# Kernel tuning notes

Measured on AMD Instinct MI355X. Metric: run time of the kernel, lower is better.

The kernel has to match this reference:

```python
import jax, jax.numpy as jnp
import numpy as np

NUM_SAMPLES = 64
PE_FREQS = 10
HIDDEN = 256
IN_PE = 3 + 3 * 2 * PE_FREQS  # 63


def positional_encoding(x):
    # x: [..., 3] -> [..., 63]
    freqs = 2.0 ** jnp.arange(PE_FREQS, dtype=x.dtype)  # [L]
    xb = x[..., None, :] * freqs[:, None]               # [..., L, 3]
    enc = jnp.concatenate([jnp.sin(xb), jnp.cos(xb)], axis=-1)  # [..., L, 6]
    return jnp.concatenate([x, enc.reshape(*x.shape[:-1], -1)], axis=-1)


def setup_inputs() -> dict:
    key = jax.random.key(0)
    ks = jax.random.split(key, 12)
    origins = jax.random.normal(ks[0], (2048, 3), dtype=jnp.float32)
    directions = jax.random.normal(ks[1], (2048, 3), dtype=jnp.float32)
    directions = directions / jnp.linalg.norm(directions, axis=-1, keepdims=True)

    def lin(kw, kb, fan_in, fan_out):
        s = 1.0 / np.sqrt(fan_in)
        W = jax.random.uniform(kw, (fan_in, fan_out), jnp.float32, -s, s)
        b = jax.random.uniform(kb, (fan_out,), jnp.float32, -s, s)
        return W, b

    W0, b0 = lin(ks[2], ks[3], IN_PE, HIDDEN)
    W1, b1 = lin(ks[4], ks[5], HIDDEN, HIDDEN)
    W2, b2 = lin(ks[6], ks[7], HIDDEN, HIDDEN)
    W3, b3 = lin(ks[8], ks[9], HIDDEN, 4)
    return {"origins": origins, "directions": directions,
            "near": 2.0, "far": 6.0,
            "W0": W0, "b0": b0, "W1": W1, "b1": b1,
            "W2": W2, "b2": b2, "W3": W3, "b3": b3}


def field_mlp(x, W0, b0, W1, b1, W2, b2, W3, b3):
    h = positional_encoding(x)
    h = jax.nn.relu(h @ W0 + b0)
    h = jax.nn.relu(h @ W1 + b1)
    h = jax.nn.relu(h @ W2 + b2)
    return h @ W3 + b3  # [..., 4]


def reference(origins, directions, near, far, W0, b0, W1, b1, W2, b2, W3, b3):
    near = jnp.float32(near)
    far = jnp.float32(far)
    # 1) sample generation (faithful to source, including its midpoint formula)
    boundaries = jnp.linspace(near, far, NUM_SAMPLES + 1)          # [S+1]
    midpoints = boundaries[:-1] + boundaries[1:] / 2               # [S] (as in source)
    samples = jnp.einsum('i,jk->jik', midpoints, directions)      # [B,S,3]
    locations = origins[:, None, :] + samples                      # [B,S,3]
    # 2) field eval (vectorized; equivalent to per-ray list comprehension)
    field_out = field_mlp(locations, W0, b0, W1, b1, W2, b2, W3, b3)  # [B,S,4]
    rgb = jax.nn.sigmoid(field_out[..., :3])                       # [B,S,3]
    sigma = jax.nn.relu(field_out[..., 3])                         # [B,S]
    # 3) alpha values
    delta = jnp.diff(boundaries)                                    # [S]
    alpha = 1.0 - jnp.exp(-sigma * delta)                           # [B,S]
    # 4) alpha composite: exclusive cumprod transmittance (O(N) form of source loop)
    trans = jnp.cumprod(1.0 - alpha, axis=1)
    T = jnp.concatenate([jnp.ones_like(alpha[:, :1]), trans[:, :-1]], axis=1)
    weights = T * alpha                                             # [B,S]
    return jnp.sum(weights[..., None] * rgb, axis=1)                # [B,3]
```

## Files before the change

### kernel.cpp

```cpp
#include <hip/hip_runtime.h>
#include <math.h>

typedef _Float16 h8 __attribute__((ext_vector_type(8)));
typedef _Float16 h4 __attribute__((ext_vector_type(4)));
typedef float    f4 __attribute__((ext_vector_type(4)));

#define SAMPLES 64
#define HIDDEN  256

#define OFF_W0 0
#define OFF_W1 16384
#define OFF_W2 81920
#define OFF_W3 147456

__launch_bounds__(256)
__global__ void prep_weights(const float* __restrict__ W0,
                             const float* __restrict__ W1,
                             const float* __restrict__ W2,
                             const float* __restrict__ W3,
                             _Float16* __restrict__ ws)
{
    const int ln = threadIdx.x & 63;
    const int t  = blockIdx.x * 4 + (threadIdx.x >> 6);
    if (t >= 296) return;

    const float* src; int off, kg, ct, kmax, colmax, wide;
    if (t < 32)       { src=W0; off=OFF_W0; kg=t>>4;        ct=t&15;        kmax=63;  colmax=256; wide=1; }
    else if (t < 160) { int u=t-32;  src=W1; off=OFF_W1; kg=u>>4; ct=u&15; kmax=256; colmax=256; wide=1; }
    else if (t < 288) { int u=t-160; src=W2; off=OFF_W2; kg=u>>4; ct=u&15; kmax=256; colmax=256; wide=1; }
    else              { int u=t-288; src=W3; off=OFF_W3; kg=u;    ct=0;    kmax=256; colmax=4;   wide=0; }

    const int col = ct*16 + (ln & 15);
    const int k0  = kg*32 + ((ln >> 4) << 3);
    h8 vh;
#pragma unroll
    for (int j = 0; j < 8; ++j) {
        int k = k0 + j;
        float v = (k < kmax && col < colmax) ? src[k*colmax + col] : 0.0f;
        vh[j] = (_Float16)v;
    }
    int di = wide ? ((kg*16 + ct)*64 + ln) : (kg*64 + ln);
    ((h8*)(ws + off))[di] = vh;
}

template<int NKG>
__device__ __forceinline__ void dense_layer(const _Float16* __restrict__ W,
                                            const float*    __restrict__ bias,
                                            _Float16* B, int wv, int lane,
                                            h8 (&ca)[2],
                                            const h8* __restrict__ next0,
                                            const h8* __restrict__ next1)
{
    const int q  = lane >> 4;
    const int jl = lane & 15;
    f4 acc[2][8];
#pragma unroll
    for (int cht = 0; cht < 2; ++cht)
#pragma unroll
        for (int st = 0; st < 8; ++st) acc[cht][st] = (f4){0.f, 0.f, 0.f, 0.f};

    const h8* wp = (const h8*)W;
    const h8* bp = (const h8*)B;

#pragma unroll
    for (int kg = 0; kg < NKG; ++kg) {
        h8 na[2];
        if (kg + 1 < NKG) {
#pragma unroll
            for (int cht = 0; cht < 2; ++cht)
                na[cht] = wp[((kg+1)*16 + wv*2 + cht)*64 + lane];
        } else {
            na[0] = *next0;
            na[1] = *next1;
        }
#pragma unroll
        for (int sh = 0; sh < 2; ++sh) {
            h8 bh[4];
#pragma unroll
            for (int s = 0; s < 4; ++s)
                bh[s] = bp[(kg*8 + sh*4 + s)*64 + lane];
#pragma unroll
            for (int s = 0; s < 4; ++s) {
                acc[0][sh*4+s] = __builtin_amdgcn_mfma_f32_16x16x32_f16(ca[0], bh[s], acc[0][sh*4+s], 0, 0, 0);
                acc[1][sh*4+s] = __builtin_amdgcn_mfma_f32_16x16x32_f16(ca[1], bh[s], acc[1][sh*4+s], 0, 0, 0);
            }
        }
        ca[0] = na[0]; ca[1] = na[1];
    }

    f4 bb0 = ((const f4*)bias)[wv*8 + q];
    f4 bb1 = ((const f4*)bias)[wv*8 + 4 + q];

    __syncthreads();

#pragma unroll
    for (int cht = 0; cht < 2; ++cht) {
        f4 bb = cht ? bb1 : bb0;
        int lnp = jl + 16*(cht*2 + (q >> 1));
        int jb  = (q & 1)*4;
#pragma unroll
        for (int st = 0; st < 8; ++st) {
            h4 vh;
#pragma unroll
            for (int r = 0; r < 4; ++r)
                vh[r] = (_Float16)fmaxf(acc[cht][st][r] + bb[r], 0.0f);
            *(h4*)(B + ((wv*8 + st)*64 + lnp)*8 + jb) = vh;
        }
    }
    __syncthreads();
}

__launch_bounds__(512, 2)
__global__ void nerf_fused(const float* __restrict__ origins,
                           const float* __restrict__ dirs,
                           const float* __restrict__ nearp,
                           const float* __restrict__ farp,
                           const float* __restrict__ b0,
                           const float* __restrict__ b1,
                           const float* __restrict__ b2,
                           const float* __restrict__ b3,
                           const _Float16* __restrict__ ws,
                           float* __restrict__ out,
                           int nrays)
{
    extern __shared__ _Float16 sm[];
    _Float16* B = sm;
    float* headv = (float*)(sm + 32768);

    const int tid  = threadIdx.x;
    const int wv   = tid >> 6;
    const int lane = tid & 63;
    const int ray0 = blockIdx.x * 2;
    const int ray1 = ray0 + 1;
    const int ray1c = (ray1 < nrays) ? ray1 : (nrays - 1);

    const int fi0 = (wv*2 + 0)*64 + lane;
    const int fi1 = (wv*2 + 1)*64 + lane;
    const h8* w0p = (const h8*)(ws + OFF_W0);
    const h8* w1p = (const h8*)(ws + OFF_W1);
    const h8* w2p = (const h8*)(ws + OFF_W2);
    const h8* w3p = (const h8*)(ws + OFF_W3);
    h8 wca[2];
    wca[0] = w0p[fi0];
    wca[1] = w0p[fi1];

    const float near = nearp[0];
    const float far  = farp[0];
    const float step = (far - near) * (1.0f / 64.0f);

    {
        const int f  = tid >> 7;
        const int sg = tid & 127;
        const int rr = sg >> 6;
        const int p  = sg & 63;
        const int st = rr*4 + (p >> 4);
        const int jl = p & 15;
        const int kg = f >> 1;
        const int q0 = (f & 1)*2;

        const float mid = (near + (float)p*step) + (near + (float)(p+1)*step)*0.5f;
        const float ox = origins[ray0*3+0], oy = origins[ray0*3+1], oz = origins[ray0*3+2];
        const float dx = dirs[ray0*3+0],    dy = dirs[ray0*3+1],    dz = dirs[ray0*3+2];
        const float o1x = origins[ray1c*3+0], o1y = origins[ray1c*3+1], o1z = origins[ray1c*3+2];
        const float d1x = dirs[ray1c*3+0],    d1y = dirs[ray1c*3+1],    d1z = dirs[ray1c*3+2];
        float c3[3];
        c3[0] = (rr ? o1x : ox) + mid*(rr ? d1x : dx);
        c3[1] = (rr ? o1y : oy) + mid*(rr ? d1y : dy);
        c3[2] = (rr ? o1z : oz) + mid*(rr ? d1z : dz);

        float ls0 = sinf(c3[0]), lc0 = cosf(c3[0]);
        float ls1 = sinf(c3[1]), lc1 = cosf(c3[1]);
        float ls2 = sinf(c3[2]), lc2 = cosf(c3[2]);
#define DBL() { float t0 = 2.f*ls0*lc0; lc0 = 1.f - 2.f*ls0*ls0; ls0 = t0; \
                float t1 = 2.f*ls1*lc1; lc1 = 1.f - 2.f*ls1*ls1; ls1 = t1; \
                float t2 = 2.f*ls2*lc2; lc2 = 1.f - 2.f*ls2*ls2; ls2 = t2; }
        h8 vh0, vh1;
        if (f == 0) {
            vh0[0]=(_Float16)c3[0]; vh0[1]=(_Float16)c3[1]; vh0[2]=(_Float16)c3[2];
            vh0[3]=(_Float16)ls0;   vh0[4]=(_Float16)ls1;   vh0[5]=(_Float16)ls2;
            vh0[6]=(_Float16)lc0;   vh0[7]=(_Float16)lc1;   vh1[0]=(_Float16)lc2;
            DBL();
            vh1[1]=(_Float16)ls0; vh1[2]=(_Float16)ls1; vh1[3]=(_Float16)ls2;
            vh1[4]=(_Float16)lc0; vh1[5]=(_Float16)lc1; vh1[6]=(_Float16)lc2;
            DBL();
            vh1[7]=(_Float16)ls0;
        } else if (f == 1) {
            DBL(); DBL();
            vh0[0]=(_Float16)ls1; vh0[1]=(_Float16)ls2;
            vh0[2]=(_Float16)lc0; vh0[3]=(_Float16)lc1; vh0[4]=(_Float16)lc2;
            DBL();
            vh0[5]=(_Float16)ls0; vh0[6]=(_Float16)ls1; vh0[7]=(_Float16)ls2;
            vh1[0]=(_Float16)lc0; vh1[1]=(_Float16)lc1; vh1[2]=(_Float16)lc2;
            DBL();
            vh1[3]=(_Float16)ls0; vh1[4]=(_Float16)ls1; vh1[5]=(_Float16)ls2;
            vh1[6]=(_Float16)lc0; vh1[7]=(_Float16)lc1;
        } else if (f == 2) {
            DBL(); DBL(); DBL(); DBL();
            vh0[0]=(_Float16)lc2;
            DBL();
            vh0[1]=(_Float16)ls0; vh0[2]=(_Float16)ls1; vh0[3]=(_Float16)ls2;
            vh0[4]=(_Float16)lc0; vh0[5]=(_Float16)lc1; vh0[6]=(_Float16)lc2;
            DBL();
            vh0[7]=(_Float16)ls0; vh1[0]=(_Float16)ls1; vh1[1]=(_Float16)ls2;
            vh1[2]=(_Float16)lc0; vh1[3]=(_Float16)lc1; vh1[4]=(_Float16)lc2;
            DBL();
            vh1[5]=(_Float16)ls0; vh1[6]=(_Float16)ls1; vh1[7]=(_Float16)ls2;
        } else {
            DBL(); DBL(); DBL(); DBL(); DBL(); DBL(); DBL();
            vh0[0]=(_Float16)lc0; vh0[1]=(_Float16)lc1; vh0[2]=(_Float16)lc2;
            DBL();
            vh0[3]=(_Float16)ls0; vh0[4]=(_Float16)ls1; vh0[5]=(_Float16)ls2;
            vh0[6]=(_Float16)lc0; vh0[7]=(_Float16)lc1; vh1[0]=(_Float16)lc2;
            DBL();
            vh1[1]=(_Float16)ls0; vh1[2]=(_Float16)ls1; vh1[3]=(_Float16)ls2;
            vh1[4]=(_Float16)lc0; vh1[5]=(_Float16)lc1; vh1[6]=(_Float16)lc2;
            vh1[7]=(_Float16)0.0f;
        }
#undef DBL
        ((h8*)B)[(kg*8 + st)*64 + (q0    )*16 + jl] = vh0;
        ((h8*)B)[(kg*8 + st)*64 + (q0 + 1)*16 + jl] = vh1;
    }
    __syncthreads();

    dense_layer<2>(ws+OFF_W0, b0, B, wv, lane, wca, &w1p[fi0], &w1p[fi1]);
    dense_layer<8>(ws+OFF_W1, b1, B, wv, lane, wca, &w2p[fi0], &w2p[fi1]);
    dense_layer<8>(ws+OFF_W2, b2, B, wv, lane, wca,
                   &w3p[wv*64 + lane], &w3p[wv*64 + lane]);

    f4 hacc[8];
    {
        h8 ah = wca[0];
        const h8* bp = (const h8*)B;
#pragma unroll
        for (int st = 0; st < 8; ++st) {
            f4 z = (f4){0.f, 0.f, 0.f, 0.f};
            hacc[st] = __builtin_amdgcn_mfma_f32_16x16x32_f16(ah, bp[(wv*8 + st)*64 + lane], z, 0, 0, 0);
        }
    }
    __syncthreads();

    f4* part = (f4*)sm;
#pragma unroll
    for (int st = 0; st < 8; ++st) part[(wv*8 + st)*64 + lane] = hacc[st];
    __syncthreads();

    {
        int stt = tid >> 6, l = tid & 63;
        f4 s = part[(0*8 + stt)*64 + l];
#pragma unroll
        for (int w = 1; w < 8; ++w) s += part[(w*8 + stt)*64 + l];
        int q = l >> 4, jl = l & 15;
        if (q == 0) {
            s += *(const f4*)b3;
            ((f4*)headv)[(stt >> 2)*64 + (stt & 3)*16 + jl] = s;
        }
    }
    __syncthreads();

    if (tid < 128) {
        const int rr = tid >> 6;
        const int p  = tid & 63;
        f4 f = ((const f4*)headv)[rr*64 + p];
        float sigma = fmaxf(f[3], 0.0f);
        float delta = (near + (float)(p + 1)*step) - (near + (float)p*step);
        float alpha = 1.0f - expf(-sigma * delta);
        float om    = 1.0f - alpha;

        float prod = om;
#pragma unroll
        for (int off = 1; off < 64; off <<= 1) {
            float v = __shfl_up(prod, off, 64);
            if (p >= off) prod *= v;
        }
        float T = __shfl_up(prod, 1, 64);
        if (p == 0) T = 1.0f;
        float w = T * alpha;

        float r  = w * (1.0f / (1.0f + expf(-f[0])));
        float g  = w * (1.0f / (1.0f + expf(-f[1])));
        float bb = w * (1.0f / (1.0f + expf(-f[2])));
#pragma unroll
        for (int off = 32; off > 0; off >>= 1) {
            r  += __shfl_down(r,  off, 64);
            g  += __shfl_down(g,  off, 64);
            bb += __shfl_down(bb, off, 64);
        }
        if (p == 0 && ray0 + rr < nrays) {
            out[(ray0 + rr)*3 + 0] = r;
            out[(ray0 + rr)*3 + 1] = g;
            out[(ray0 + rr)*3 + 2] = bb;
        }
    }
}

extern "C" void kernel_launch(void* const* d_in, const int* in_sizes, int n_in,
                              void* d_out, int out_size, void* d_ws, size_t ws_size,
                              hipStream_t stream) {
    const float* origins = (const float*)d_in[0];
    const float* dirs    = (const float*)d_in[1];
    const float* nearp   = (const float*)d_in[2];
    const float* farp    = (const float*)d_in[3];
    const float* W0      = (const float*)d_in[4];
    const float* b0      = (const float*)d_in[5];
    const float* W1      = (const float*)d_in[6];
    const float* b1      = (const float*)d_in[7];
    const float* W2      = (const float*)d_in[8];
    const float* b2      = (const float*)d_in[9];
    const float* W3      = (const float*)d_in[10];
    const float* b3      = (const float*)d_in[11];
    float* out           = (float*)d_out;
    _Float16* ws         = (_Float16*)d_ws;

    const int nrays = in_sizes[0] / 3;
    const int nblk  = (nrays + 1) / 2;

    prep_weights<<<dim3(74), dim3(256), 0, stream>>>(W0, W1, W2, W3, ws);

    const size_t shmem = 32768 * sizeof(_Float16) + 128 * sizeof(f4);
    hipFuncSetAttribute(reinterpret_cast<const void*>(nerf_fused),
                        hipFuncAttributeMaxDynamicSharedMemorySize,
                        (int)shmem);
    nerf_fused<<<dim3(nblk), dim3(512), shmem, stream>>>(
        origins, dirs, nearp, farp, b0, b1, b2, b3, ws, out, nrays);
}
```

Measured before the change: 118.3 us.

## Split each block's MLP work across 16 waves instead of 8

Doubles the block to 1024 threads so each wave handles half the sample tiles (4 instead of 8) for its column group. The positional encoding setup is split so each thread writes one vector instead of two. This halves the accumulator registers per wave and adds more waves to hide latency. In exchange, the block-wide barriers now cover more waves, each wave loads the same weight fragments redundantly, and occupancy drops to one block per CU.

```diff
diff --git a/kernel.cpp b/kernel.cpp
--- a/kernel.cpp
+++ b/kernel.cpp
@@ -46,18 +46,18 @@
 template<int NKG>
 __device__ __forceinline__ void dense_layer(const _Float16* __restrict__ W,
                                             const float*    __restrict__ bias,
-                                            _Float16* B, int wv, int lane,
+                                            _Float16* B, int cg, int stbase, int lane,
                                             h8 (&ca)[2],
                                             const h8* __restrict__ next0,
                                             const h8* __restrict__ next1)
 {
     const int q  = lane >> 4;
     const int jl = lane & 15;
-    f4 acc[2][8];
+    f4 acc[2][4];
 #pragma unroll
     for (int cht = 0; cht < 2; ++cht)
 #pragma unroll
-        for (int st = 0; st < 8; ++st) acc[cht][st] = (f4){0.f, 0.f, 0.f, 0.f};
+        for (int s = 0; s < 4; ++s) acc[cht][s] = (f4){0.f, 0.f, 0.f, 0.f};
 
     const h8* wp = (const h8*)W;
     const h8* bp = (const h8*)B;
@@ -68,28 +68,25 @@
         if (kg + 1 < NKG) {
 #pragma unroll
             for (int cht = 0; cht < 2; ++cht)
-                na[cht] = wp[((kg+1)*16 + wv*2 + cht)*64 + lane];
+                na[cht] = wp[((kg+1)*16 + cg*2 + cht)*64 + lane];
         } else {
             na[0] = *next0;
             na[1] = *next1;
         }
-#pragma unroll
-        for (int sh = 0; sh < 2; ++sh) {
-            h8 bh[4];
-#pragma unroll
-            for (int s = 0; s < 4; ++s)
-                bh[s] = bp[(kg*8 + sh*4 + s)*64 + lane];
-#pragma unroll
-            for (int s = 0; s < 4; ++s) {
-                acc[0][sh*4+s] = __builtin_amdgcn_mfma_f32_16x16x32_f16(ca[0], bh[s], acc[0][sh*4+s], 0, 0, 0);
-                acc[1][sh*4+s] = __builtin_amdgcn_mfma_f32_16x16x32_f16(ca[1], bh[s], acc[1][sh*4+s], 0, 0, 0);
-            }
+        h8 bh[4];
+#pragma unroll
+        for (int s = 0; s < 4; ++s)
+            bh[s] = bp[(kg*8 + stbase + s)*64 + lane];
+#pragma unroll
+        for (int s = 0; s < 4; ++s) {
+            acc[0][s] = __builtin_amdgcn_mfma_f32_16x16x32_f16(ca[0], bh[s], acc[0][s], 0, 0, 0);
+            acc[1][s] = __builtin_amdgcn_mfma_f32_16x16x32_f16(ca[1], bh[s], acc[1][s], 0, 0, 0);
         }
         ca[0] = na[0]; ca[1] = na[1];
     }
 
-    f4 bb0 = ((const f4*)bias)[wv*8 + q];
-    f4 bb1 = ((const f4*)bias)[wv*8 + 4 + q];
+    f4 bb0 = ((const f4*)bias)[cg*8 + q];
+    f4 bb1 = ((const f4*)bias)[cg*8 + 4 + q];
 
     __syncthreads();
 
@@ -99,18 +96,18 @@
         int lnp = jl + 16*(cht*2 + (q >> 1));
         int jb  = (q & 1)*4;
 #pragma unroll
-        for (int st = 0; st < 8; ++st) {
+        for (int s = 0; s < 4; ++s) {
             h4 vh;
 #pragma unroll
             for (int r = 0; r < 4; ++r)
-                vh[r] = (_Float16)fmaxf(acc[cht][st][r] + bb[r], 0.0f);
-            *(h4*)(B + ((wv*8 + st)*64 + lnp)*8 + jb) = vh;
+                vh[r] = (_Float16)fmaxf(acc[cht][s][r] + bb[r], 0.0f);
+            *(h4*)(B + ((cg*8 + stbase + s)*64 + lnp)*8 + jb) = vh;
         }
     }
     __syncthreads();
 }
 
-__launch_bounds__(512, 2)
+__launch_bounds__(1024, 1)
 __global__ void nerf_fused(const float* __restrict__ origins,
                            const float* __restrict__ dirs,
                            const float* __restrict__ nearp,
@@ -130,33 +127,37 @@
     const int tid  = threadIdx.x;
     const int wv   = tid >> 6;
     const int lane = tid & 63;
+    const int cg     = wv >> 1;
+    const int stbase = (wv & 1) * 4;
     const int ray0 = blockIdx.x * 2;
     const int ray1 = ray0 + 1;
     const int ray1c = (ray1 < nrays) ? ray1 : (nrays - 1);
 
-    const int fi0 = (wv*2 + 0)*64 + lane;
-    const int fi1 = (wv*2 + 1)*64 + lane;
+    const int f10 = (cg*2 + 0)*64 + lane;
+    const int f11 = (cg*2 + 1)*64 + lane;
     const h8* w0p = (const h8*)(ws + OFF_W0);
     const h8* w1p = (const h8*)(ws + OFF_W1);
     const h8* w2p = (const h8*)(ws + OFF_W2);
     const h8* w3p = (const h8*)(ws + OFF_W3);
     h8 wca[2];
-    wca[0] = w0p[fi0];
-    wca[1] = w0p[fi1];
+    wca[0] = w0p[f10];
+    wca[1] = w0p[f11];
 
     const float near = nearp[0];
     const float far  = farp[0];
     const float step = (far - near) * (1.0f / 64.0f);
 
     {
-        const int f  = tid >> 7;
-        const int sg = tid & 127;
+        const int o   = tid >> 7;
+        const int fp  = o >> 1;
+        const int sub = o & 1;
+        const int sg  = tid & 127;
         const int rr = sg >> 6;
         const int p  = sg & 63;
         const int st = rr*4 + (p >> 4);
         const int jl = p & 15;
-        const int kg = f >> 1;
-        const int q0 = (f & 1)*2;
+        const int kg = fp >> 1;
+        const int q0 = (fp & 1)*2;
 
         const float mid = (near + (float)p*step) + (near + (float)(p+1)*step)*0.5f;
         const float ox = origins[ray0*3+0], oy = origins[ray0*3+1], oz = origins[ray0*3+2];
@@ -175,7 +176,7 @@
                 float t1 = 2.f*ls1*lc1; lc1 = 1.f - 2.f*ls1*ls1; ls1 = t1; \
                 float t2 = 2.f*ls2*lc2; lc2 = 1.f - 2.f*ls2*ls2; ls2 = t2; }
         h8 vh0, vh1;
-        if (f == 0) {
+        if (fp == 0) {
             vh0[0]=(_Float16)c3[0]; vh0[1]=(_Float16)c3[1]; vh0[2]=(_Float16)c3[2];
             vh0[3]=(_Float16)ls0;   vh0[4]=(_Float16)ls1;   vh0[5]=(_Float16)ls2;
             vh0[6]=(_Float16)lc0;   vh0[7]=(_Float16)lc1;   vh1[0]=(_Float16)lc2;
@@ -184,7 +185,7 @@
             vh1[4]=(_Float16)lc0; vh1[5]=(_Float16)lc1; vh1[6]=(_Float16)lc2;
             DBL();
             vh1[7]=(_Float16)ls0;
-        } else if (f == 1) {
+        } else if (fp == 1) {
             DBL(); DBL();
             vh0[0]=(_Float16)ls1; vh0[1]=(_Float16)ls2;
             vh0[2]=(_Float16)lc0; vh0[3]=(_Float16)lc1; vh0[4]=(_Float16)lc2;
@@ -194,7 +195,7 @@
             DBL();
             vh1[3]=(_Float16)ls0; vh1[4]=(_Float16)ls1; vh1[5]=(_Float16)ls2;
             vh1[6]=(_Float16)lc0; vh1[7]=(_Float16)lc1;
-        } else if (f == 2) {
+        } else if (fp == 2) {
             DBL(); DBL(); DBL(); DBL();
             vh0[0]=(_Float16)lc2;
             DBL();
@@ -217,34 +218,33 @@
             vh1[7]=(_Float16)0.0f;
         }
 #undef DBL
-        ((h8*)B)[(kg*8 + st)*64 + (q0    )*16 + jl] = vh0;
-        ((h8*)B)[(kg*8 + st)*64 + (q0 + 1)*16 + jl] = vh1;
-    }
-    __syncthreads();
-
-    dense_layer<2>(ws+OFF_W0, b0, B, wv, lane, wca, &w1p[fi0], &w1p[fi1]);
-    dense_layer<8>(ws+OFF_W1, b1, B, wv, lane, wca, &w2p[fi0], &w2p[fi1]);
-    dense_layer<8>(ws+OFF_W2, b2, B, wv, lane, wca,
-                   &w3p[wv*64 + lane], &w3p[wv*64 + lane]);
-
-    f4 hacc[8];
+        ((h8*)B)[(kg*8 + st)*64 + (q0 + sub)*16 + jl] = sub ? vh1 : vh0;
+    }
+    __syncthreads();
+
+    dense_layer<2>(ws+OFF_W0, b0, B, cg, stbase, lane, wca, &w1p[f10], &w1p[f11]);
+    dense_layer<8>(ws+OFF_W1, b1, B, cg, stbase, lane, wca, &w2p[f10], &w2p[f11]);
+    dense_layer<8>(ws+OFF_W2, b2, B, cg, stbase, lane, wca,
+                   &w3p[cg*64 + lane], &w3p[cg*64 + lane]);
+
+    f4 hacc[4];
     {
         h8 ah = wca[0];
         const h8* bp = (const h8*)B;
 #pragma unroll
-        for (int st = 0; st < 8; ++st) {
+        for (int s = 0; s < 4; ++s) {
             f4 z = (f4){0.f, 0.f, 0.f, 0.f};
-            hacc[st] = __builtin_amdgcn_mfma_f32_16x16x32_f16(ah, bp[(wv*8 + st)*64 + lane], z, 0, 0, 0);
+            hacc[s] = __builtin_amdgcn_mfma_f32_16x16x32_f16(ah, bp[(cg*8 + stbase + s)*64 + lane], z, 0, 0, 0);
         }
     }
     __syncthreads();
 
     f4* part = (f4*)sm;
 #pragma unroll
-    for (int st = 0; st < 8; ++st) part[(wv*8 + st)*64 + lane] = hacc[st];
-    __syncthreads();
-
-    {
+    for (int s = 0; s < 4; ++s) part[(cg*8 + stbase + s)*64 + lane] = hacc[s];
+    __syncthreads();
+
+    if (tid < 512) {
         int stt = tid >> 6, l = tid & 63;
         f4 s = part[(0*8 + stt)*64 + l];
 #pragma unroll
@@ -320,6 +320,6 @@
     hipFuncSetAttribute(reinterpret_cast<const void*>(nerf_fused),
                         hipFuncAttributeMaxDynamicSharedMemorySize,
                         (int)shmem);
-    nerf_fused<<<dim3(nblk), dim3(512), shmem, stream>>>(
+    nerf_fused<<<dim3(nblk), dim3(1024), shmem, stream>>>(
         origins, dirs, nearp, farp, b0, b1, b2, b3, ws, out, nrays);
 }
```

After: 124.0 us. +4.8%, slower.
